# Optimization experiments

Hardware: AMD Instinct MI355X
Metric: run time of the kernel (lower is better)

The kernel has to match this reference:

```python
import jax, jax.numpy as jnp
import numpy as np

B, HW, C, H = 4, 2048, 768, 8
HD = C // H  # 96


def _rotate_half_interleaved(t):
    # t: [..., HD]; pairs (t1, t2) at even/odd positions -> (-t2, t1) interleaved
    t1 = t[..., ::2]
    t2 = t[..., 1::2]
    return jnp.stack([-t2, t1], axis=-1).reshape(t.shape)


def setup_inputs() -> dict:
    key = jax.random.key(0)
    kx, kq, kp, kb = jax.random.split(key, 4)
    x = jax.random.normal(kx, (B, HW, C), dtype=jnp.float32)
    # standard interleaved RoPE tables: freq repeated pairwise along head_dim
    inv_freq = 1.0 / (10000.0 ** (np.arange(0, HD, 2, dtype=np.float32) / HD))  # [HD/2]
    angles = np.arange(HW, dtype=np.float32)[:, None] * inv_freq[None, :]        # [HW, HD/2]
    angles = np.repeat(angles, 2, axis=-1)                                        # [HW, HD]
    cos = jnp.asarray(np.cos(angles), dtype=jnp.float32)
    sin = jnp.asarray(np.sin(angles), dtype=jnp.float32)
    Wqkv = jax.random.normal(kq, (3 * C, C), dtype=jnp.float32) * (C ** -0.5)
    Wproj = jax.random.normal(kp, (C, C), dtype=jnp.float32) * (C ** -0.5)
    bproj = jnp.zeros((C,), dtype=jnp.float32)
    return {"x": x, "cos": cos, "sin": sin, "Wqkv": Wqkv, "Wproj": Wproj, "bproj": bproj}


def reference(x, cos, sin, Wqkv, Wproj, bproj):
    Bv, hw, Cv = x.shape
    scale = HD ** -0.5
    qkv = x @ Wqkv.T                                  # [B, hw, 3C]
    qkv = qkv.reshape(Bv, hw, 3, H, HD).transpose(2, 0, 3, 1, 4)  # [3, B, H, hw, HD]
    q, k, v = qkv[0], qkv[1], qkv[2]
    # RoPE: broadcast cos/sin [hw, HD] over [B, H, hw, HD]
    cosb = cos[None, None, :, :]
    sinb = sin[None, None, :, :]
    q = q * cosb + _rotate_half_interleaved(q) * sinb
    k = k * cosb + _rotate_half_interleaved(k) * sinb
    attn = jnp.einsum('bhqd,bhkd->bhqk', q, k) * scale
    attn = jax.nn.softmax(attn, axis=-1)
    out = jnp.einsum('bhqk,bhkd->bhqd', attn, v)      # [B, H, hw, HD]
    out = out.transpose(0, 2, 1, 3).reshape(Bv, hw, Cv)
    return out @ Wproj.T + bproj
```

## Files before the change

### kernel.cpp

```cpp
#include <hip/hip_runtime.h>
#include <hip/hip_bf16.h>
#include <math.h>

#define Bc  4
#define HWc 2048
#define Cc  768
#define Hc  8
#define HDc 96

typedef short bf16x8 __attribute__((ext_vector_type(8)));
typedef float f32x4  __attribute__((ext_vector_type(4)));

static __device__ __forceinline__ unsigned short f2bf(float x) {
    __hip_bfloat16 h = __float2bfloat16(x);
    return *reinterpret_cast<unsigned short*>(&h);
}

#define GLOBAL_AS(p) ((const __attribute__((address_space(1))) void*)(p))
#define LDS_AS(p)    ((__attribute__((address_space(3))) void*)(p))

__global__ __launch_bounds__(256) void cast_all(
    const float* __restrict__ x, const float* __restrict__ Wq,
    const float* __restrict__ Wp, unsigned short* __restrict__ xb,
    unsigned short* __restrict__ Wqb, unsigned short* __restrict__ Wpb,
    int nx4, int nwq4, int nwp4)
{
    int i = blockIdx.x * 256 + threadIdx.x;
    const float* src; unsigned short* dst; int j = i;
    if (i < nx4) { src = x; dst = xb; }
    else if ((j = i - nx4) < nwq4) { src = Wq; dst = Wqb; }
    else if ((j = i - nx4 - nwq4) < nwp4) { src = Wp; dst = Wpb; }
    else return;
    float4 v = ((const float4*)src)[j];
    ushort4 p;
    p.x = f2bf(v.x); p.y = f2bf(v.y); p.z = f2bf(v.z); p.w = f2bf(v.w);
    ((ushort4*)dst)[j] = p;
}

__global__ __launch_bounds__(256) void qkv_mfma_T(
    const unsigned short* __restrict__ Wb, const unsigned short* __restrict__ xb,
    const float* __restrict__ cs, const float* __restrict__ sn,
    unsigned short* __restrict__ qo, unsigned short* __restrict__ ko,
    unsigned short* __restrict__ vt)
{
    __shared__ unsigned short Al[128 * 32];
    __shared__ unsigned short Bl[128 * 32];
    __shared__ unsigned short Tt[64][132];
    const int tid  = threadIdx.x;
    const int lane = tid & 63;
    const int w    = tid >> 6;
    const int c    = lane & 15, qd = lane >> 4;
    const int wm   = w & 1, wn = w >> 1;
    const int m0   = blockIdx.y << 7;
    const int n0   = blockIdx.x << 7;

    const int srow = (w << 5) + (lane >> 2);
    const int sseg = (lane & 3) << 3;
    const unsigned short* Ag = Wb + (size_t)(m0 + srow) * Cc + sseg;
    const unsigned short* Bg = xb + (size_t)(n0 + srow) * Cc + sseg;
    unsigned short* Adst = &Al[(w << 5) * 32];
    unsigned short* Bdst = &Bl[(w << 5) * 32];

    f32x4 acc[4][4];
    #pragma unroll
    for (int i = 0; i < 4; i++)
        #pragma unroll
        for (int j = 0; j < 4; j++) acc[i][j] = (f32x4)0.f;

    for (int k0 = 0; k0 < Cc; k0 += 32) {
        __syncthreads();
        __builtin_amdgcn_global_load_lds(GLOBAL_AS(Ag + k0),            LDS_AS(Adst),            16, 0, 0);
        __builtin_amdgcn_global_load_lds(GLOBAL_AS(Ag + 16 * Cc + k0),  LDS_AS(Adst + 16 * 32),  16, 0, 0);
        __builtin_amdgcn_global_load_lds(GLOBAL_AS(Bg + k0),            LDS_AS(Bdst),            16, 0, 0);
        __builtin_amdgcn_global_load_lds(GLOBAL_AS(Bg + 16 * Cc + k0),  LDS_AS(Bdst + 16 * 32),  16, 0, 0);
        __syncthreads();

        bf16x8 af[4], bfr[4];
        #pragma unroll
        for (int mt = 0; mt < 4; mt++)
            af[mt] = *(const bf16x8*)&Al[((wm << 6) + mt * 16 + c) * 32 + qd * 8];
        #pragma unroll
        for (int nt = 0; nt < 4; nt++)
            bfr[nt] = *(const bf16x8*)&Bl[((wn << 6) + nt * 16 + c) * 32 + qd * 8];
        #pragma unroll
        for (int mt = 0; mt < 4; mt++)
            #pragma unroll
            for (int nt = 0; nt < 4; nt++)
                acc[mt][nt] = __builtin_amdgcn_mfma_f32_16x16x32_bf16(
                    af[mt], bfr[nt], acc[mt][nt], 0, 0, 0);
    }

    const int which = m0 / Cc;
    const int m0l = m0 - which * Cc;
    const float qs = 0.10206207261596577f;

    if (which == 2) {
        #pragma unroll
        for (int mt = 0; mt < 4; mt++) {
            const int c0 = m0l + (wm << 6) + mt * 16 + (qd << 2);
            const int h = c0 / HDc, d = c0 % HDc;
            #pragma unroll
            for (int nt = 0; nt < 4; nt++) {
                const int t = n0 + (wn << 6) + nt * 16 + c;
                const int b = t >> 11, tt = t & (HWc - 1);
                const size_t base = ((size_t)((b * Hc + h) * HDc + d)) * HWc + tt;
                #pragma unroll
                for (int r = 0; r < 4; r++)
                    vt[base + (size_t)r * HWc] = f2bf(acc[mt][nt][r]);
            }
        }
    } else {
        unsigned short* dst = which ? ko : qo;
        const float sc = which ? 1.0f : qs;
        for (int tk = 0; tk < 2; tk++) {
            __syncthreads();
            if (wn == tk) {
                #pragma unroll
                for (int mt = 0; mt < 4; mt++) {
                    const int c0 = m0l + (wm << 6) + mt * 16 + (qd << 2);
                    const int d = c0 % HDc;
                    #pragma unroll
                    for (int nt = 0; nt < 4; nt++) {
                        const int t = n0 + (wn << 6) + nt * 16 + c;
                        const int tt = t & (HWc - 1);
                        const float4 c4 = *(const float4*)&cs[tt * HDc + d];
                        const float4 s4 = *(const float4*)&sn[tt * HDc + d];
                        float o0 = (acc[mt][nt][0] * c4.x - acc[mt][nt][1] * s4.x) * sc;
                        float o1 = (acc[mt][nt][1] * c4.y + acc[mt][nt][0] * s4.y) * sc;
                        float o2 = (acc[mt][nt][2] * c4.z - acc[mt][nt][3] * s4.z) * sc;
                        float o3 = (acc[mt][nt][3] * c4.w + acc[mt][nt][2] * s4.w) * sc;
                        ushort4 pk;
                        pk.x = f2bf(o0); pk.y = f2bf(o1);
                        pk.z = f2bf(o2); pk.w = f2bf(o3);
                        *(ushort4*)&Tt[nt * 16 + c][(wm << 6) + mt * 16 + (qd << 2)] = pk;
                    }
                }
            }
            __syncthreads();
            #pragma unroll
            for (int it = 0; it < 8; it++) {
                int s = tid + (it << 8);
                int row = s >> 5, fseg = (s & 31) << 2;
                int fg = m0l + fseg;
                int h = fg / HDc, d = fg % HDc;
                int token = n0 + tk * 64 + row;
                int b = token >> 11, tt = token & (HWc - 1);
                *(ushort4*)&dst[((size_t)(b * Hc + h) * HWc + tt) * HDc + d] =
                    *(ushort4*)&Tt[row][fseg];
            }
        }
    }
}

__global__ __launch_bounds__(256, 4) void attn_flash(
    const unsigned short* __restrict__ qg, const unsigned short* __restrict__ kg,
    const unsigned short* __restrict__ vtg, unsigned short* __restrict__ ob)
{
    __shared__ unsigned short Ks[64][104];
    __shared__ unsigned short Vt[96][72];
    __shared__ unsigned short Pt[4][16][72];

    const int tid  = threadIdx.x;
    const int lane = tid & 63;
    const int w    = tid >> 6;
    const int c    = lane & 15;
    const int qd   = lane >> 4;
    const int bh   = blockIdx.x;
    const int b    = bh >> 3, h = bh & 7;
    const int q0   = blockIdx.y << 6;

    const unsigned short* kb  = kg  + (size_t)bh * HWc * HDc;
    const unsigned short* vtb = vtg + (size_t)bh * HDc * HWc;

    bf16x8 qt[3];
    {
        const unsigned short* qr = qg + ((size_t)bh * HWc + q0 + w * 16 + c) * HDc + qd * 8;
        #pragma unroll
        for (int ks = 0; ks < 3; ks++)
            qt[ks] = *(const bf16x8*)(qr + ks * 32);
    }

    f32x4 oacc[6];
    #pragma unroll
    for (int mt = 0; mt < 6; mt++) oacc[mt] = (f32x4)0.f;
    float lsum = 0.f;

    for (int ck = 0; ck < 32; ck++) {
        __syncthreads();
        {
            const unsigned short* kc = kb + (size_t)(ck << 6) * HDc;
            #pragma unroll
            for (int it = 0; it < 3; it++) {
                int idx = tid + (it << 8);
                int row = idx / 12, seg = idx - row * 12;
                uint4 val = *(const uint4*)(kc + row * HDc + seg * 8);
                *(uint4*)&Ks[row][seg * 8] = val;
            }
            const unsigned short* vc = vtb + (ck << 6);
            #pragma unroll
            for (int it = 0; it < 3; it++) {
                int idx = tid + (it << 8);
                int row = idx >> 3, seg = idx & 7;
                uint4 val = *(const uint4*)(vc + (size_t)row * HWc + seg * 8);
                *(uint4*)&Vt[row][seg * 8] = val;
            }
        }
        __syncthreads();

        f32x4 sacc[4];
        #pragma unroll
        for (int mt = 0; mt < 4; mt++) sacc[mt] = (f32x4)0.f;
        #pragma unroll
        for (int mt = 0; mt < 4; mt++)
            #pragma unroll
            for (int ks = 0; ks < 3; ks++) {
                bf16x8 af = *(const bf16x8*)&Ks[mt * 16 + c][ks * 32 + qd * 8];
                sacc[mt] = __builtin_amdgcn_mfma_f32_16x16x32_bf16(
                    af, qt[ks], sacc[mt], 0, 0, 0);
            }

        float rs = 0.f;
        #pragma unroll
        for (int mt = 0; mt < 4; mt++)
            #pragma unroll
            for (int r = 0; r < 4; r++) {
                float p = __expf(sacc[mt][r]);
                sacc[mt][r] = p;
                rs += p;
            }
        rs += __shfl_xor(rs, 16);
        rs += __shfl_xor(rs, 32);
        lsum += rs;

        #pragma unroll
        for (int mt = 0; mt < 4; mt++) {
            __hip_bfloat162 p01 = __float22bfloat162_rn(float2{sacc[mt][0], sacc[mt][1]});
            __hip_bfloat162 p23 = __float22bfloat162_rn(float2{sacc[mt][2], sacc[mt][3]});
            uint2 pk;
            pk.x = *reinterpret_cast<unsigned int*>(&p01);
            pk.y = *reinterpret_cast<unsigned int*>(&p23);
            *(uint2*)&Pt[w][c][mt * 16 + qd * 4] = pk;
        }
        bf16x8 pf[2];
        #pragma unroll
        for (int ks = 0; ks < 2; ks++)
            pf[ks] = *(const bf16x8*)&Pt[w][c][ks * 32 + qd * 8];

        #pragma unroll
        for (int mt = 0; mt < 6; mt++)
            #pragma unroll
            for (int ks = 0; ks < 2; ks++) {
                bf16x8 vf = *(const bf16x8*)&Vt[mt * 16 + c][ks * 32 + qd * 8];
                oacc[mt] = __builtin_amdgcn_mfma_f32_16x16x32_bf16(
                    vf, pf[ks], oacc[mt], 0, 0, 0);
            }
    }

    const float linv = 1.0f / lsum;
    unsigned short* orow = ob + ((size_t)(b * HWc + q0 + w * 16 + c)) * Cc + h * HDc;
    #pragma unroll
    for (int mt = 0; mt < 6; mt++) {
        f32x4 val = oacc[mt] * linv;
        ushort4 pk;
        pk.x = f2bf(val[0]); pk.y = f2bf(val[1]);
        pk.z = f2bf(val[2]); pk.w = f2bf(val[3]);
        *(ushort4*)&orow[mt * 16 + qd * 4] = pk;
    }
}

__global__ __launch_bounds__(256) void proj_mfma_T64(
    const unsigned short* __restrict__ Wb, const unsigned short* __restrict__ Ab,
    const float* __restrict__ bias, float* __restrict__ out)
{
    __shared__ unsigned short Al[128 * 32];
    __shared__ unsigned short Bl[64 * 32];
    const int tid  = threadIdx.x;
    const int lane = tid & 63;
    const int w    = tid >> 6;
    const int c    = lane & 15, qd = lane >> 4;
    const int wm   = w & 1, wn = w >> 1;
    const int m0   = blockIdx.y << 7;
    const int n0   = blockIdx.x << 6;

    const int srow = (w << 5) + (lane >> 2);
    const int sseg = (lane & 3) << 3;
    const unsigned short* Ag = Wb + (size_t)(m0 + srow) * Cc + sseg;
    unsigned short* Adst = &Al[(w << 5) * 32];
    const int brow = (w << 4) + (lane >> 2);
    const unsigned short* Bg = Ab + (size_t)(n0 + brow) * Cc + sseg;
    unsigned short* Bdst = &Bl[(w << 4) * 32];

    f32x4 acc[4][2];
    #pragma unroll
    for (int i = 0; i < 4; i++)
        #pragma unroll
        for (int j = 0; j < 2; j++) acc[i][j] = (f32x4)0.f;

    for (int k0 = 0; k0 < Cc; k0 += 32) {
        __syncthreads();
        __builtin_amdgcn_global_load_lds(GLOBAL_AS(Ag + k0),           LDS_AS(Adst),           16, 0, 0);
        __builtin_amdgcn_global_load_lds(GLOBAL_AS(Ag + 16 * Cc + k0), LDS_AS(Adst + 16 * 32), 16, 0, 0);
        __builtin_amdgcn_global_load_lds(GLOBAL_AS(Bg + k0),           LDS_AS(Bdst),           16, 0, 0);
        __syncthreads();

        bf16x8 af[4], bfr[2];
        #pragma unroll
        for (int mt = 0; mt < 4; mt++)
            af[mt] = *(const bf16x8*)&Al[((wm << 6) + mt * 16 + c) * 32 + qd * 8];
        #pragma unroll
        for (int nt = 0; nt < 2; nt++)
            bfr[nt] = *(const bf16x8*)&Bl[((wn << 5) + nt * 16 + c) * 32 + qd * 8];
        #pragma unroll
        for (int mt = 0; mt < 4; mt++)
            #pragma unroll
            for (int nt = 0; nt < 2; nt++)
                acc[mt][nt] = __builtin_amdgcn_mfma_f32_16x16x32_bf16(
                    af[mt], bfr[nt], acc[mt][nt], 0, 0, 0);
    }

    #pragma unroll
    for (int mt = 0; mt < 4; mt++) {
        const int f = m0 + (wm << 6) + mt * 16 + (qd << 2);
        const float4 b4 = *(const float4*)&bias[f];
        #pragma unroll
        for (int nt = 0; nt < 2; nt++) {
            const int t = n0 + (wn << 5) + nt * 16 + c;
            float4 val;
            val.x = acc[mt][nt][0] + b4.x;
            val.y = acc[mt][nt][1] + b4.y;
            val.z = acc[mt][nt][2] + b4.z;
            val.w = acc[mt][nt][3] + b4.w;
            *(float4*)&out[(size_t)t * Cc + f] = val;
        }
    }
}

extern "C" void kernel_launch(void* const* d_in, const int* in_sizes, int n_in,
                              void* d_out, int out_size, void* d_ws, size_t ws_size,
                              hipStream_t stream) {
    const float* x     = (const float*)d_in[0];
    const float* cs    = (const float*)d_in[1];
    const float* sn    = (const float*)d_in[2];
    const float* Wqkv  = (const float*)d_in[3];
    const float* Wproj = (const float*)d_in[4];
    const float* bproj = (const float*)d_in[5];
    float* out = (float*)d_out;

    const size_t per = (size_t)Bc * Hc * HWc * HDc;
    const size_t nx  = per;
    const size_t nwq = (size_t)3 * Cc * Cc;
    const size_t nwp = (size_t)Cc * Cc;

    unsigned short* xb  = (unsigned short*)d_ws;
    unsigned short* Wqb = xb + nx;
    unsigned short* Wpb = Wqb + nwq;
    unsigned short* q   = Wpb + nwp;
    unsigned short* k   = q + per;
    unsigned short* vt  = k + per;
    unsigned short* ob  = vt + per;

    const int nx4 = (int)(nx / 4), nwq4 = (int)(nwq / 4), nwp4 = (int)(nwp / 4);
    const int ntot = nx4 + nwq4 + nwp4;
    cast_all<<<dim3((ntot + 255) / 256), 256, 0, stream>>>(
        x, Wqkv, Wproj, xb, Wqb, Wpb, nx4, nwq4, nwp4);

    qkv_mfma_T<<<dim3(64, 18), 256, 0, stream>>>(Wqb, xb, cs, sn, q, k, vt);
    attn_flash<<<dim3(32, 32), 256, 0, stream>>>(q, k, vt, ob);
    proj_mfma_T64<<<dim3(128, 6), 256, 0, stream>>>(Wpb, ob, bproj, out);
}
```

Before: 284.7 us.

## Process two 16-row query subtiles per wave to reuse K/V fragments

Each attention block now handles 128 queries instead of 64: every wave computes two 16-query subtiles, so each K and V fragment read from LDS and each global K/V tile load feeds twice the MFMA work. The grid halves along the query axis and launch bounds drop to 2 blocks per SM to leave room for the doubled accumulators. The cost is higher register pressure, lower occupancy, and only 512 blocks, which may leave compute units underused on this GPU.

```diff
diff --git a/kernel.cpp b/kernel.cpp
--- a/kernel.cpp
+++ b/kernel.cpp
@@ -152,13 +152,13 @@
     }
 }
 
-__global__ __launch_bounds__(256, 4) void attn_flash(
+__global__ __launch_bounds__(256, 2) void attn_flash(
     const unsigned short* __restrict__ qg, const unsigned short* __restrict__ kg,
     const unsigned short* __restrict__ vtg, unsigned short* __restrict__ ob)
 {
     __shared__ unsigned short Ks[64][104];
     __shared__ unsigned short Vt[96][72];
-    __shared__ unsigned short Pt[4][16][72];
+    __shared__ unsigned short Pt[4][16][136];
 
     const int tid  = threadIdx.x;
     const int lane = tid & 63;
@@ -167,23 +167,27 @@
     const int qd   = lane >> 4;
     const int bh   = blockIdx.x;
     const int b    = bh >> 3, h = bh & 7;
-    const int q0   = blockIdx.y << 6;
+    const int q0   = blockIdx.y << 7;
 
     const unsigned short* kb  = kg  + (size_t)bh * HWc * HDc;
     const unsigned short* vtb = vtg + (size_t)bh * HDc * HWc;
 
-    bf16x8 qt[3];
-    {
-        const unsigned short* qr = qg + ((size_t)bh * HWc + q0 + w * 16 + c) * HDc + qd * 8;
+    bf16x8 qt[2][3];
+    #pragma unroll
+    for (int s = 0; s < 2; s++) {
+        const unsigned short* qr =
+            qg + ((size_t)bh * HWc + q0 + (w << 5) + (s << 4) + c) * HDc + (qd << 3);
         #pragma unroll
         for (int ks = 0; ks < 3; ks++)
-            qt[ks] = *(const bf16x8*)(qr + ks * 32);
-    }
-
-    f32x4 oacc[6];
-    #pragma unroll
-    for (int mt = 0; mt < 6; mt++) oacc[mt] = (f32x4)0.f;
-    float lsum = 0.f;
+            qt[s][ks] = *(const bf16x8*)(qr + ks * 32);
+    }
+
+    f32x4 oacc[2][6];
+    #pragma unroll
+    for (int s = 0; s < 2; s++)
+        #pragma unroll
+        for (int mt = 0; mt < 6; mt++) oacc[s][mt] = (f32x4)0.f;
+    float lsum[2] = {0.f, 0.f};
 
     for (int ck = 0; ck < 32; ck++) {
         __syncthreads();
@@ -207,64 +211,79 @@
         }
         __syncthreads();
 
-        f32x4 sacc[4];
-        #pragma unroll
-        for (int mt = 0; mt < 4; mt++) sacc[mt] = (f32x4)0.f;
+        f32x4 sacc[2][4];
+        #pragma unroll
+        for (int s = 0; s < 2; s++)
+            #pragma unroll
+            for (int mt = 0; mt < 4; mt++) sacc[s][mt] = (f32x4)0.f;
         #pragma unroll
         for (int mt = 0; mt < 4; mt++)
             #pragma unroll
             for (int ks = 0; ks < 3; ks++) {
                 bf16x8 af = *(const bf16x8*)&Ks[mt * 16 + c][ks * 32 + qd * 8];
-                sacc[mt] = __builtin_amdgcn_mfma_f32_16x16x32_bf16(
-                    af, qt[ks], sacc[mt], 0, 0, 0);
-            }
-
-        float rs = 0.f;
-        #pragma unroll
-        for (int mt = 0; mt < 4; mt++)
-            #pragma unroll
-            for (int r = 0; r < 4; r++) {
-                float p = __expf(sacc[mt][r]);
-                sacc[mt][r] = p;
-                rs += p;
-            }
-        rs += __shfl_xor(rs, 16);
-        rs += __shfl_xor(rs, 32);
-        lsum += rs;
-
-        #pragma unroll
-        for (int mt = 0; mt < 4; mt++) {
-            __hip_bfloat162 p01 = __float22bfloat162_rn(float2{sacc[mt][0], sacc[mt][1]});
-            __hip_bfloat162 p23 = __float22bfloat162_rn(float2{sacc[mt][2], sacc[mt][3]});
-            uint2 pk;
-            pk.x = *reinterpret_cast<unsigned int*>(&p01);
-            pk.y = *reinterpret_cast<unsigned int*>(&p23);
-            *(uint2*)&Pt[w][c][mt * 16 + qd * 4] = pk;
-        }
-        bf16x8 pf[2];
-        #pragma unroll
-        for (int ks = 0; ks < 2; ks++)
-            pf[ks] = *(const bf16x8*)&Pt[w][c][ks * 32 + qd * 8];
+                sacc[0][mt] = __builtin_amdgcn_mfma_f32_16x16x32_bf16(
+                    af, qt[0][ks], sacc[0][mt], 0, 0, 0);
+                sacc[1][mt] = __builtin_amdgcn_mfma_f32_16x16x32_bf16(
+                    af, qt[1][ks], sacc[1][mt], 0, 0, 0);
+            }
+
+        #pragma unroll
+        for (int s = 0; s < 2; s++) {
+            float rs = 0.f;
+            #pragma unroll
+            for (int mt = 0; mt < 4; mt++)
+                #pragma unroll
+                for (int r = 0; r < 4; r++) {
+                    float p = __expf(sacc[s][mt][r]);
+                    sacc[s][mt][r] = p;
+                    rs += p;
+                }
+            rs += __shfl_xor(rs, 16);
+            rs += __shfl_xor(rs, 32);
+            lsum[s] += rs;
+
+            #pragma unroll
+            for (int mt = 0; mt < 4; mt++) {
+                __hip_bfloat162 p01 = __float22bfloat162_rn(float2{sacc[s][mt][0], sacc[s][mt][1]});
+                __hip_bfloat162 p23 = __float22bfloat162_rn(float2{sacc[s][mt][2], sacc[s][mt][3]});
+                uint2 pk;
+                pk.x = *reinterpret_cast<unsigned int*>(&p01);
+                pk.y = *reinterpret_cast<unsigned int*>(&p23);
+                *(uint2*)&Pt[w][c][(s << 6) + mt * 16 + (qd << 2)] = pk;
+            }
+        }
+        bf16x8 pf[2][2];
+        #pragma unroll
+        for (int s = 0; s < 2; s++)
+            #pragma unroll
+            for (int ks = 0; ks < 2; ks++)
+                pf[s][ks] = *(const bf16x8*)&Pt[w][c][(s << 6) + ks * 32 + (qd << 3)];
 
         #pragma unroll
         for (int mt = 0; mt < 6; mt++)
             #pragma unroll
             for (int ks = 0; ks < 2; ks++) {
                 bf16x8 vf = *(const bf16x8*)&Vt[mt * 16 + c][ks * 32 + qd * 8];
-                oacc[mt] = __builtin_amdgcn_mfma_f32_16x16x32_bf16(
-                    vf, pf[ks], oacc[mt], 0, 0, 0);
-            }
-    }
-
-    const float linv = 1.0f / lsum;
-    unsigned short* orow = ob + ((size_t)(b * HWc + q0 + w * 16 + c)) * Cc + h * HDc;
-    #pragma unroll
-    for (int mt = 0; mt < 6; mt++) {
-        f32x4 val = oacc[mt] * linv;
-        ushort4 pk;
-        pk.x = f2bf(val[0]); pk.y = f2bf(val[1]);
-        pk.z = f2bf(val[2]); pk.w = f2bf(val[3]);
-        *(ushort4*)&orow[mt * 16 + qd * 4] = pk;
+                oacc[0][mt] = __builtin_amdgcn_mfma_f32_16x16x32_bf16(
+                    vf, pf[0][ks], oacc[0][mt], 0, 0, 0);
+                oacc[1][mt] = __builtin_amdgcn_mfma_f32_16x16x32_bf16(
+                    vf, pf[1][ks], oacc[1][mt], 0, 0, 0);
+            }
+    }
+
+    #pragma unroll
+    for (int s = 0; s < 2; s++) {
+        const float linv = 1.0f / lsum[s];
+        unsigned short* orow =
+            ob + ((size_t)(b * HWc + q0 + (w << 5) + (s << 4) + c)) * Cc + h * HDc;
+        #pragma unroll
+        for (int mt = 0; mt < 6; mt++) {
+            f32x4 val = oacc[s][mt] * linv;
+            ushort4 pk;
+            pk.x = f2bf(val[0]); pk.y = f2bf(val[1]);
+            pk.z = f2bf(val[2]); pk.w = f2bf(val[3]);
+            *(ushort4*)&orow[mt * 16 + (qd << 2)] = pk;
+        }
     }
 }
 
@@ -365,6 +384,6 @@
         x, Wqkv, Wproj, xb, Wqb, Wpb, nx4, nwq4, nwp4);
 
     qkv_mfma_T<<<dim3(64, 18), 256, 0, stream>>>(Wqb, xb, cs, sn, q, k, vt);
-    attn_flash<<<dim3(32, 32), 256, 0, stream>>>(q, k, vt, ob);
+    attn_flash<<<dim3(32, 16), 256, 0, stream>>>(q, k, vt, ob);
     proj_mfma_T64<<<dim3(128, 6), 256, 0, stream>>>(Wpb, ob, bproj, out);
 }
```

After: 304.8 us. 7.1% more time.

## Register-prefetch next K/V chunk during compute and raise MFMA wave priority

Applied to the files above, without the earlier changes.

The attention kernel now loads the next 64-row K and V^T chunk from global memory into registers while the current chunk is being computed. Those registers are written to LDS at the start of the next iteration, so global latency overlaps the MFMA work instead of stalling between barriers. It also wraps the two MFMA loops in s_setprio to favour matrix-issuing waves. The cost is extra VGPRs for the staged tiles and a redundant reload on the last iteration, which may lower occupancy.

```diff
diff --git a/kernel.cpp b/kernel.cpp
--- a/kernel.cpp
+++ b/kernel.cpp
@@ -180,36 +180,50 @@
             qt[ks] = *(const bf16x8*)(qr + ks * 32);
     }
 
+    int krow[3], kseg[3], vrow[3], vseg[3];
+    #pragma unroll
+    for (int it = 0; it < 3; it++) {
+        int idx = tid + (it << 8);
+        krow[it] = idx / 12; kseg[it] = idx - krow[it] * 12;
+        vrow[it] = idx >> 3; vseg[it] = idx & 7;
+    }
+
     f32x4 oacc[6];
     #pragma unroll
     for (int mt = 0; mt < 6; mt++) oacc[mt] = (f32x4)0.f;
     float lsum = 0.f;
 
+    uint4 kreg[3], vreg[3];
+    #pragma unroll
+    for (int it = 0; it < 3; it++) {
+        kreg[it] = *(const uint4*)(kb + (size_t)krow[it] * HDc + kseg[it] * 8);
+        vreg[it] = *(const uint4*)(vtb + (size_t)vrow[it] * HWc + vseg[it] * 8);
+    }
+
     for (int ck = 0; ck < 32; ck++) {
         __syncthreads();
+        #pragma unroll
+        for (int it = 0; it < 3; it++) {
+            *(uint4*)&Ks[krow[it]][kseg[it] * 8] = kreg[it];
+            *(uint4*)&Vt[vrow[it]][vseg[it] * 8] = vreg[it];
+        }
+        __syncthreads();
+
         {
-            const unsigned short* kc = kb + (size_t)(ck << 6) * HDc;
+            const int nk = (ck < 31) ? ck + 1 : 31;
+            const unsigned short* kc = kb + (size_t)(nk << 6) * HDc;
+            const unsigned short* vc = vtb + (nk << 6);
             #pragma unroll
             for (int it = 0; it < 3; it++) {
-                int idx = tid + (it << 8);
-                int row = idx / 12, seg = idx - row * 12;
-                uint4 val = *(const uint4*)(kc + row * HDc + seg * 8);
-                *(uint4*)&Ks[row][seg * 8] = val;
-            }
-            const unsigned short* vc = vtb + (ck << 6);
-            #pragma unroll
-            for (int it = 0; it < 3; it++) {
-                int idx = tid + (it << 8);
-                int row = idx >> 3, seg = idx & 7;
-                uint4 val = *(const uint4*)(vc + (size_t)row * HWc + seg * 8);
-                *(uint4*)&Vt[row][seg * 8] = val;
-            }
-        }
-        __syncthreads();
+                kreg[it] = *(const uint4*)(kc + (size_t)krow[it] * HDc + kseg[it] * 8);
+                vreg[it] = *(const uint4*)(vc + (size_t)vrow[it] * HWc + vseg[it] * 8);
+            }
+        }
 
         f32x4 sacc[4];
         #pragma unroll
         for (int mt = 0; mt < 4; mt++) sacc[mt] = (f32x4)0.f;
+        __builtin_amdgcn_s_setprio(1);
         #pragma unroll
         for (int mt = 0; mt < 4; mt++)
             #pragma unroll
@@ -218,6 +232,7 @@
                 sacc[mt] = __builtin_amdgcn_mfma_f32_16x16x32_bf16(
                     af, qt[ks], sacc[mt], 0, 0, 0);
             }
+        __builtin_amdgcn_s_setprio(0);
 
         float rs = 0.f;
         #pragma unroll
@@ -246,6 +261,7 @@
         for (int ks = 0; ks < 2; ks++)
             pf[ks] = *(const bf16x8*)&Pt[w][c][ks * 32 + qd * 8];
 
+        __builtin_amdgcn_s_setprio(1);
         #pragma unroll
         for (int mt = 0; mt < 6; mt++)
             #pragma unroll
@@ -254,6 +270,7 @@
                 oacc[mt] = __builtin_amdgcn_mfma_f32_16x16x32_bf16(
                     vf, pf[ks], oacc[mt], 0, 0, 0);
             }
+        __builtin_amdgcn_s_setprio(0);
     }
 
     const float linv = 1.0f / lsum;
```

Measured after the change: 414.5 us. 1.46x slower.
